# Optimization experiments

Hardware: AMD Instinct MI355X
Metric: run time of the kernel (lower is better)

## Reference

```python
import jax, jax.numpy as jnp
import numpy as np

V, E, H, L, S, B = 32000, 1024, 512, 2, 512, 32  # vocab, emb dim, per-dir hidden, layers, seq, batch
PAD = 0
assert E == 2 * H  # required by the module's pred_emb shape assert; lets cell weights stack


def setup_inputs() -> dict:
    ks = iter(jax.random.split(jax.random.key(0), 40))
    def nrm(shape, scale=0.05):
        return jax.random.normal(next(ks), shape, dtype=jnp.float32) * scale
    seq_input = jax.random.randint(next(ks), (S, B), 1, V)
    # lengths sorted descending (pack_padded convention the torch code assumes)
    lengths = jnp.sort(jax.random.randint(next(ks), (B,), S // 2, S + 1))[::-1]
    inp = {"seq_input": seq_input, "lengths": lengths}
    for name in ("emb1", "emb2", "emb3"):
        inp[name] = nrm((V, E)).at[PAD].set(0.0)  # padding_idx row is zero
    inp["W_et"] = nrm((H, E)); inp["b_et"] = nrm((H,))      # embedding_transform
    inp["W_ct"] = nrm((H, H)); inp["b_ct"] = nrm((H,))      # context_transform
    inp["W_sc"] = nrm((1, H)); inp["b_sc"] = nrm((1,))      # to_scalar
    inp["W_g"] = nrm((E, 2 * E)); inp["b_g"] = nrm((E,))    # embedding_gate Linear
    inp["h0f"] = jax.random.uniform(next(ks), (H,), jnp.float32)  # torch.rand init params
    inp["c0f"] = jax.random.uniform(next(ks), (H,), jnp.float32)
    inp["h0b"] = jax.random.uniform(next(ks), (H,), jnp.float32)
    inp["c0b"] = jax.random.uniform(next(ks), (H,), jnp.float32)
    # LSTMCell weights: [layer, dir(fwd,bwd), 4H, in]; in==E==2H for all layers
    inp["Wih"] = nrm((L, 2, 4 * H, E))
    inp["Whh"] = nrm((L, 2, 4 * H, H))
    inp["bih"] = nrm((L, 2, 4 * H))
    inp["bhh"] = nrm((L, 2, 4 * H))
    return inp


def _lstm_cell(x, h, c, Wih, Whh, bih, bhh):
    g = x @ Wih.T + h @ Whh.T + bih + bhh
    i, f, gg, o = jnp.split(g, 4, axis=-1)
    c2 = jax.nn.sigmoid(f) * c + jax.nn.sigmoid(i) * jnp.tanh(gg)
    return jax.nn.sigmoid(o) * jnp.tanh(c2), c2


def _reverse_seq(x, lengths):
    # reverse the first `length` timesteps per batch element, keep padding in place
    t = jnp.arange(x.shape[0])[:, None]
    idx = jnp.where(t < lengths[None, :], lengths[None, :] - 1 - t, t)  # [S,B]
    idx = idx.reshape(idx.shape + (1,) * (x.ndim - 2))
    return jnp.take_along_axis(x, jnp.broadcast_to(idx, x.shape), axis=0)


def _cos(a, b):
    n = jnp.sum(a * b, -1)
    d = jnp.maximum(jnp.linalg.norm(a, axis=-1) * jnp.linalg.norm(b, axis=-1), 1e-8)
    return n / d


def _forward(seq_input, lengths, emb1, emb2, emb3, W_et, b_et, W_ct, b_ct, W_sc, b_sc,
             W_g, b_g, h0f, c0f, h0b, c0b, Wih, Whh, bih, bhh):
    Sl, Bn = seq_input.shape
    Hh = Whh.shape[-1]
    nL = Wih.shape[0]
    # active mask at step t: lengths >= t+1 (identical for forward and reversed scans)
    mask = jnp.arange(Sl)[:, None] < lengths[None, :]  # [S,B]
    h0f_b = jnp.broadcast_to(h0f, (Bn, Hh)); c0f_b = jnp.broadcast_to(c0f, (Bn, Hh))
    h0b_b = jnp.broadcast_to(h0b, (Bn, Hh)); c0b_b = jnp.broadcast_to(c0b, (Bn, Hh))
    cell = lambda l, d: (Wih[l, d], Whh[l, d], bih[l, d], bhh[l, d])

    def layer0_scan(tokens, cell_p, h0, c0):
        def step(carry, inp):
            h, c, pen = carry
            tok, m = inp
            e1, e2, e3 = emb1[tok], emb2[tok], emb3[tok]  # [B,E]
            p = (jax.nn.relu(_cos(e1, e2) - 0.3) + jax.nn.relu(_cos(e1, e3) - 0.3)
                 + jax.nn.relu(_cos(e2, e3) - 0.3))
            pen = pen + jnp.sum(jnp.where(m, p, 0.0))
            ctx = h @ W_ct.T + b_ct  # [B,H]
            sc = lambda e: jnp.tanh(e @ W_et.T + b_et + ctx) @ W_sc.T + b_sc  # [B,1]
            w = jax.nn.softmax(jnp.concatenate([sc(e1), sc(e2), sc(e3)], -1), axis=-1)
            x = w[:, :1] * e1 + w[:, 1:2] * e2 + w[:, 2:3] * e3  # attended embedding
            h2, c2 = _lstm_cell(x, h, c, *cell_p)
            mm = m[:, None]
            h = jnp.where(mm, h2, h)
            c = jnp.where(mm, c2, c)
            return (h, c, pen), (jnp.where(mm, h2, 0.0), jnp.where(mm, x, 0.0))
        (hf, cf, pen), (outs, preds) = jax.lax.scan(
            step, (h0, c0, jnp.zeros((), jnp.float32)), (tokens, mask))
        return hf, cf, outs, pen, preds

    def layer_scan(xs, cell_p, h0, c0):
        def step(carry, inp):
            h, c = carry
            x, m = inp
            h2, c2 = _lstm_cell(x, h, c, *cell_p)
            mm = m[:, None]
            return (jnp.where(mm, h2, h), jnp.where(mm, c2, c)), jnp.where(mm, h2, 0.0)
        (hf, cf), outs = jax.lax.scan(step, (h0, c0), (xs, mask))
        return hf, cf, outs

    # layer 0 with embedding attention + cosine penalty
    hF, cF, outF, penF, predF = layer0_scan(seq_input, cell(0, 0), h0f_b, c0f_b)
    hB, cB, outB, penB, predB = layer0_scan(_reverse_seq(seq_input, lengths), cell(0, 1), h0b_b, c0b_b)
    penalty = penF + penB
    predB = _reverse_seq(predB, lengths)
    gate = jax.nn.sigmoid(jnp.concatenate([predF, predB], -1) @ W_g.T + b_g)
    pred_emb = predF * gate + predB * (1.0 - gate)
    x = jnp.concatenate([outF, _reverse_seq(outB, lengths)], -1)  # [S,B,2H]
    hs = [hF, hB]; cs = [cF, cB]
    for l in range(1, nL):
        hF, cF, oF = layer_scan(x, cell(l, 0), h0f_b, c0f_b)
        hB, cB, oB = layer_scan(_reverse_seq(x, lengths), cell(l, 1), h0b_b, c0b_b)
        x = jnp.concatenate([oF, _reverse_seq(oB, lengths)], -1)
        hs += [hF, hB]; cs += [cF, cB]
    final_h = jnp.stack(hs, 0)  # [2L,B,H]
    final_c = jnp.stack(cs, 0)
    return final_h, final_c, x, penalty, pred_emb


def reference(seq_input, lengths, emb1, emb2, emb3, W_et, b_et, W_ct, b_ct, W_sc, b_sc,
              W_g, b_g, h0f, c0f, h0b, c0b, Wih, Whh, bih, bhh):
    return _forward(seq_input, lengths, emb1, emb2, emb3, W_et, b_et, W_ct, b_ct, W_sc,
                    b_sc, W_g, b_g, h0f, c0f, h0b, c0b, Wih, Whh, bih, bhh)
```

## Files before the change

### kernel.cpp

```cpp
#include <hip/hip_runtime.h>

typedef unsigned short u16;
typedef unsigned long long u64;
typedef __bf16 bf16_t;
typedef bf16_t bf16x8 __attribute__((ext_vector_type(8)));
typedef float f32x4 __attribute__((ext_vector_type(4)));

#define DEVFN static __device__ __forceinline__

constexpr int S_ = 512, B_ = 32, H_ = 512, E_ = 1024;
constexpr int SB_ = S_ * B_;

constexpr size_t OUT_FH  = 0;
constexpr size_t OUT_FC  = 65536;
constexpr size_t OUT_X   = 131072;
constexpr size_t OUT_PEN = 16908288;
constexpr size_t OUT_PE  = 16908289;

constexpr size_t WS_SLOTS = 0;
constexpr size_t WS_PEN   = 16384;
constexpr size_t WS_SPART = 16640;
constexpr size_t WS_HG0   = 41216;
constexpr size_t WS_HG1   = 106752;
constexpr size_t WS_WET   = 237824;
constexpr size_t WS_WCT   = 1286400;
constexpr size_t WS_WIH0  = 1810688;
constexpr size_t WS_WHH0  = 10199296;
constexpr size_t WS_WIH1  = 14393600;
constexpr size_t WS_WHH1  = 22782208;
constexpr size_t WS_WG    = 26976512;
constexpr size_t WS_EK    = 31170816;
constexpr size_t WS_ET    = 131834112;
constexpr size_t WS_PREDF = 232497408;
constexpr size_t WS_PREDB = 266051840;
constexpr size_t WS_OUT0F = 299606272;
constexpr size_t WS_OUT0B = 316383488;

DEVFN u16 f2bf(float f) {
  union { float f; unsigned u; } v; v.f = f;
  unsigned u = v.u;
  unsigned r = (u + 0x7fffu + ((u >> 16) & 1u)) >> 16;
  return (u16)r;
}
DEVFN float bf2f(u16 h) {
  union { unsigned u; float f; } v; v.u = ((unsigned)h) << 16;
  return v.f;
}
DEVFN float sigm(float x) { return 1.f / (1.f + __expf(-x)); }
DEVFN float tanh_f(float x) { float e = __expf(2.f * x); return 1.f - 2.f / (e + 1.f); }
DEVFN bf16x8 ld_bf8(const u16* p) { return *reinterpret_cast<const bf16x8*>(p); }
DEVFN f32x4 mfma_bf(bf16x8 a, bf16x8 b, f32x4 c) {
  return __builtin_amdgcn_mfma_f32_16x16x32_bf16(a, b, c, 0, 0, 0);
}
DEVFN void lds_st16(u16* base, int row, int rowBytes, int byteCol, bf16x8 v) {
  *reinterpret_cast<bf16x8*>((char*)base + row * rowBytes + (byteCol ^ ((row & 7) << 4))) = v;
}
DEVFN void lds_st8(u16* base, int row, int rowBytes, int byteCol, u64 v) {
  *reinterpret_cast<u64*>((char*)base + row * rowBytes + (byteCol ^ ((row & 7) << 4))) = v;
}
DEVFN bf16x8 lds_ld16(const u16* base, int row, int rowBytes, int byteCol) {
  return *reinterpret_cast<const bf16x8*>((const char*)base + row * rowBytes + (byteCol ^ ((row & 7) << 4)));
}

DEVFN u64 coh_ld64(const u64* p) {
  return __hip_atomic_load(p, __ATOMIC_RELAXED, __HIP_MEMORY_SCOPE_AGENT);
}
DEVFN void coh_st64(u64* p, u64 v) {
  __hip_atomic_store(p, v, __ATOMIC_RELAXED, __HIP_MEMORY_SCOPE_AGENT);
}
DEVFN void coh_st32(unsigned* p, unsigned v) {
  __hip_atomic_store(p, v, __ATOMIC_RELAXED, __HIP_MEMORY_SCOPE_AGENT);
}

DEVFN void gbar_arrive(unsigned* slots, int r, unsigned target) {
  __syncthreads();
  if (threadIdx.x == 0)
    __hip_atomic_store(slots + r * 16, target, __ATOMIC_RELAXED, __HIP_MEMORY_SCOPE_AGENT);
}
DEVFN void gbar_wait(unsigned* slots, unsigned target) {
  if (threadIdx.x < 64) {
    while (__hip_atomic_load(slots + threadIdx.x * 16, __ATOMIC_RELAXED,
                             __HIP_MEMORY_SCOPE_AGENT) < target)
      __builtin_amdgcn_s_sleep(1);
  }
  __syncthreads();
}
DEVFN void gbar(unsigned* slots, int r, unsigned target) {
  gbar_arrive(slots, r, target);
  gbar_wait(slots, target);
}

__global__ void k_f2bf(const float* __restrict__ src, u16* __restrict__ dst, int n) {
  for (int i = blockIdx.x * blockDim.x + threadIdx.x; i < n; i += gridDim.x * blockDim.x)
    dst[i] = f2bf(src[i]);
}

__global__ __launch_bounds__(256) void k_gather(
    const int* __restrict__ seq, const int* __restrict__ lengths,
    const float* __restrict__ emb1, const float* __restrict__ emb2, const float* __restrict__ emb3,
    u16* __restrict__ eK, float* __restrict__ pen) {
  int s = blockIdx.x;
  int t = s >> 5, b = s & 31;
  int tid = threadIdx.x;
  int tok = seq[s];
  const float4* p1 = (const float4*)(emb1 + (size_t)tok * 1024);
  const float4* p2 = (const float4*)(emb2 + (size_t)tok * 1024);
  const float4* p3 = (const float4*)(emb3 + (size_t)tok * 1024);
  float4 a = p1[tid], c = p2[tid], d = p3[tid];
  size_t rb = (size_t)s * 1024 + tid * 4;
  uint2 pk;
  pk.x = f2bf(a.x) | ((unsigned)f2bf(a.y) << 16); pk.y = f2bf(a.z) | ((unsigned)f2bf(a.w) << 16);
  *(uint2*)(eK + rb) = pk;
  pk.x = f2bf(c.x) | ((unsigned)f2bf(c.y) << 16); pk.y = f2bf(c.z) | ((unsigned)f2bf(c.w) << 16);
  *(uint2*)(eK + (size_t)SB_ * 1024 + rb) = pk;
  pk.x = f2bf(d.x) | ((unsigned)f2bf(d.y) << 16); pk.y = f2bf(d.z) | ((unsigned)f2bf(d.w) << 16);
  *(uint2*)(eK + (size_t)2 * SB_ * 1024 + rb) = pk;
  float v[6];
  v[0] = a.x*c.x + a.y*c.y + a.z*c.z + a.w*c.w;
  v[1] = a.x*d.x + a.y*d.y + a.z*d.z + a.w*d.w;
  v[2] = c.x*d.x + c.y*d.y + c.z*d.z + c.w*d.w;
  v[3] = a.x*a.x + a.y*a.y + a.z*a.z + a.w*a.w;
  v[4] = c.x*c.x + c.y*c.y + c.z*c.z + c.w*c.w;
  v[5] = d.x*d.x + d.y*d.y + d.z*d.z + d.w*d.w;
  for (int i = 0; i < 6; ++i)
    for (int m = 1; m < 64; m <<= 1) v[i] += __shfl_xor(v[i], m);
  __shared__ float red[4][6];
  int wid = tid >> 6, lane = tid & 63;
  if (lane == 0) for (int i = 0; i < 6; ++i) red[wid][i] = v[i];
  __syncthreads();
  if (tid == 0) {
    float r[6];
    for (int i = 0; i < 6; ++i) r[i] = red[0][i] + red[1][i] + red[2][i] + red[3][i];
    float c12 = r[0] / fmaxf(sqrtf(r[3]) * sqrtf(r[4]), 1e-8f);
    float c13 = r[1] / fmaxf(sqrtf(r[3]) * sqrtf(r[5]), 1e-8f);
    float c23 = r[2] / fmaxf(sqrtf(r[4]) * sqrtf(r[5]), 1e-8f);
    float p = fmaxf(c12 - 0.3f, 0.f) + fmaxf(c13 - 0.3f, 0.f) + fmaxf(c23 - 0.3f, 0.f);
    if (t < lengths[b] && p > 0.f) atomicAdd(pen, 2.f * p);
  }
}

__global__ __launch_bounds__(256) void k_gemm_et(
    const u16* __restrict__ A, const u16* __restrict__ Bw,
    const float* __restrict__ bias, float* __restrict__ C) {
  int bm = blockIdx.x % 384, bn = blockIdx.x / 384;
  int m0 = bm * 128, n0 = bn * 128;
  __shared__ u16 sA[128 * 64], sB[128 * 64];
  int tid = threadIdx.x, wid = tid >> 6, lane = tid & 63;
  int wm = wid & 1, wn = wid >> 1;
  f32x4 acc[4][4] = {};
  for (int kb = 0; kb < 16; ++kb) {
    __syncthreads();
    for (int c = tid; c < 1024; c += 256) {
      int row = c >> 3, q = c & 7;
      lds_st16(sA, row, 128, q * 16, ld_bf8(A + (size_t)(m0 + row) * 1024 + kb * 64 + q * 8));
      lds_st16(sB, row, 128, q * 16, ld_bf8(Bw + (size_t)(n0 + row) * 1024 + kb * 64 + q * 8));
    }
    __syncthreads();
    for (int kk = 0; kk < 2; ++kk) {
      bf16x8 af[4], bf[4];
      int bc = kk * 64 + (lane >> 4) * 16;
      for (int i = 0; i < 4; ++i) {
        af[i] = lds_ld16(sA, wm * 64 + i * 16 + (lane & 15), 128, bc);
        bf[i] = lds_ld16(sB, wn * 64 + i * 16 + (lane & 15), 128, bc);
      }
      for (int i = 0; i < 4; ++i)
        for (int j = 0; j < 4; ++j) acc[i][j] = mfma_bf(af[i], bf[j], acc[i][j]);
    }
  }
  for (int i = 0; i < 4; ++i)
    for (int j = 0; j < 4; ++j) {
      int m = m0 + wm * 64 + i * 16 + (lane >> 4) * 4;
      int n = n0 + wn * 64 + j * 16 + (lane & 15);
      float bn_ = bias[n & 511];
      for (int r = 0; r < 4; ++r) C[(size_t)(m + r) * 512 + n] = acc[i][j][r] + bn_;
    }
}

__global__ __launch_bounds__(256) void k_gemm_gate(
    const u16* __restrict__ pF, const u16* __restrict__ pB, const u16* __restrict__ Wg,
    const float* __restrict__ bias, float* __restrict__ outPE) {
  int bm = blockIdx.x % 128, bn = blockIdx.x / 128;
  int m0 = bm * 128, n0 = bn * 128;
  __shared__ u16 sA[128 * 64], sB[128 * 64];
  int tid = threadIdx.x, wid = tid >> 6, lane = tid & 63;
  int wm = wid & 1, wn = wid >> 1;
  f32x4 acc[4][4] = {};
  for (int kb = 0; kb < 32; ++kb) {
    __syncthreads();
    const u16* Asrc = (kb < 16) ? pF : pB;
    int kof = (kb < 16) ? kb * 64 : (kb - 16) * 64;
    for (int c = tid; c < 1024; c += 256) {
      int row = c >> 3, q = c & 7;
      lds_st16(sA, row, 128, q * 16, ld_bf8(Asrc + (size_t)(m0 + row) * 1024 + kof + q * 8));
      lds_st16(sB, row, 128, q * 16, ld_bf8(Wg + (size_t)(n0 + row) * 2048 + kb * 64 + q * 8));
    }
    __syncthreads();
    for (int kk = 0; kk < 2; ++kk) {
      bf16x8 af[4], bf[4];
      int bc = kk * 64 + (lane >> 4) * 16;
      for (int i = 0; i < 4; ++i) {
        af[i] = lds_ld16(sA, wm * 64 + i * 16 + (lane & 15), 128, bc);
        bf[i] = lds_ld16(sB, wn * 64 + i * 16 + (lane & 15), 128, bc);
      }
      for (int i = 0; i < 4; ++i)
        for (int j = 0; j < 4; ++j) acc[i][j] = mfma_bf(af[i], bf[j], acc[i][j]);
    }
  }
  for (int i = 0; i < 4; ++i)
    for (int j = 0; j < 4; ++j) {
      int m = m0 + wm * 64 + i * 16 + (lane >> 4) * 4;
      int n = n0 + wn * 64 + j * 16 + (lane & 15);
      float bn_ = bias[n];
      for (int r = 0; r < 4; ++r) {
        float g = sigm(acc[i][j][r] + bn_);
        size_t idx = (size_t)(m + r) * 1024 + n;
        float a = bf2f(pF[idx]), b = bf2f(pB[idx]);
        outPE[idx] = a * g + b * (1.f - g);
      }
    }
}

__global__ __launch_bounds__(256, 1) void k_scan0(
    const u16* __restrict__ eK, const float* __restrict__ eT,
    const u16* __restrict__ wIh0, const u16* __restrict__ wHh0, const u16* __restrict__ wCt,
    const float* __restrict__ Wsc, const float* __restrict__ bct,
    const float* __restrict__ bih, const float* __restrict__ bhh,
    const int* __restrict__ lengths,
    const float* __restrict__ h0f, const float* __restrict__ c0f,
    const float* __restrict__ h0b, const float* __restrict__ c0b,
    u16* __restrict__ hg, float* __restrict__ spart,
    u16* __restrict__ out0F, u16* __restrict__ out0B,
    u16* __restrict__ predF, u16* __restrict__ predB,
    float* __restrict__ dout, unsigned* __restrict__ slots) {
  const int dir = blockIdx.x >> 6;
  const int r   = blockIdx.x & 63;
  const int tid = threadIdx.x, wid = tid >> 6, lane = tid & 63;

  const u16* Wih = wIh0 + (size_t)dir * 2048 * 1024;
  const u16* Whh = wHh0 + (size_t)dir * 2048 * 512;
  const float* bi = bih + dir * 2048;
  const float* bh = bhh + dir * 2048;
  u16* out0 = dir ? out0B : out0F;
  u16* predD = dir ? predB : predF;
  const float* h0 = dir ? h0b : h0f;
  const float* c0 = dir ? c0b : c0f;
  u16* myhg = hg + (size_t)dir * 32 * 512;
  float* spartD = spart + (size_t)dir * 3 * 32 * 32;
  unsigned* slotg = slots + dir * 64 * 16;

  __shared__ u16 sWih[32 * 1024];
  __shared__ u16 sWhh[32 * 512];
  __shared__ u16 sH[32 * 512];
  __shared__ u16 sHpub[256];
  __shared__ float sPW[3][32][32];
  __shared__ float sHW[32][32];
  __shared__ float sSK[3][32];
  __shared__ float sWt[32][4];
  __shared__ float sBias[32];

  for (int c = tid; c < 4096; c += 256) {
    int ln = c >> 7, q = c & 127;
    int n = (ln >> 3) * 512 + r * 8 + (ln & 7);
    lds_st16(sWih, ln, 2048, q * 16, ld_bf8(Wih + (size_t)n * 1024 + q * 8));
  }
  for (int c = tid; c < 2048; c += 256) {
    int ln = c >> 6, q = c & 63;
    int n = (ln >> 3) * 512 + r * 8 + (ln & 7);
    lds_st16(sWhh, ln, 1024, q * 16, ld_bf8(Whh + (size_t)n * 512 + q * 8));
  }
  if (tid < 32) {
    int n = (tid >> 3) * 512 + r * 8 + (tid & 7);
    sBias[tid] = bi[n] + bh[n];
  }

  const int pb = tid >> 3, pj = tid & 7;
  const int gj = r * 8 + pj;
  float hreg = h0[gj], creg = c0[gj];
  const int lenb = lengths[pb];
  const int Lmax = lengths[0];

  const int Mt = wid & 1, Nt = wid >> 1;
  const int arow = Mt * 16 + (lane & 15);
  const int lenrow = lengths[arow];
  const int kq = lane >> 4;
  const int colN = Nt * 16 + (lane & 15);
  const bool isctx = (r < 32) && (wid < 2);
  int lctx[4];
  if (isctx)
    for (int reg = 0; reg < 4; ++reg) lctx[reg] = lengths[Mt * 16 + kq * 4 + reg];

  sHpub[tid] = f2bf(hreg);
  __syncthreads();
  if (tid < 64) {
    u64 v = *reinterpret_cast<const u64*>(sHpub + tid * 4);
    coh_st64((u64*)myhg + (size_t)(tid >> 1) * 128 + r * 2 + (tid & 1), v);
  }
  unsigned rnd = 0;
  gbar(slotg, r, ++rnd);

  for (int t = 0; t < Lmax; ++t) {
    const bool last = (t == Lmax - 1);
    {
      const u64* src = (const u64*)myhg;
      u64 hv[16];
#pragma unroll
      for (int i = 0; i < 16; ++i) hv[i] = coh_ld64(src + tid + i * 256);
#pragma unroll
      for (int i = 0; i < 16; ++i) {
        int c = tid + i * 256, row = c >> 7, q = c & 127;
        lds_st8(sH, row, 1024, q * 8, hv[i]);
      }
    }
    __syncthreads();
    {
      f32x4 acc = {0.f, 0.f, 0.f, 0.f};
#pragma unroll 4
      for (int kb = 0; kb < 16; ++kb) {
        bf16x8 a = lds_ld16(sH, arow, 1024, (kb * 32 + kq * 8) * 2);
        bf16x8 b = lds_ld16(sWhh, colN, 1024, (kb * 32 + kq * 8) * 2);
        acc = mfma_bf(a, b, acc);
      }
      int rb = Mt * 16 + kq * 4;
      for (int reg = 0; reg < 4; ++reg) sHW[rb + reg][colN] = acc[reg];
    }
    if (isctx) {
      f32x4 acc = {0.f, 0.f, 0.f, 0.f};
      int j = r * 16 + (lane & 15);
      const u16* Wctp = wCt + (size_t)j * 512;
#pragma unroll 4
      for (int kb = 0; kb < 16; ++kb) {
        bf16x8 a = lds_ld16(sH, arow, 1024, (kb * 32 + kq * 8) * 2);
        bf16x8 b = ld_bf8(Wctp + kb * 32 + kq * 8);
        acc = mfma_bf(a, b, acc);
      }
      float wsc = Wsc[j], bctj = bct[j];
      float part[3][4];
      for (int reg = 0; reg < 4; ++reg) {
        int b = Mt * 16 + kq * 4 + reg;
        int lb = lctx[reg];
        int pos = (dir == 0) ? t : ((t < lb) ? (lb - 1 - t) : t);
        float ctx = acc[reg] + bctj;
        size_t rowoff = (size_t)(pos * 32 + b) * 512 + j;
        for (int k = 0; k < 3; ++k)
          part[k][reg] = tanh_f(eT[(size_t)k * SB_ * 512 + rowoff] + ctx) * wsc;
      }
      for (int k = 0; k < 3; ++k)
        for (int reg = 0; reg < 4; ++reg) {
          float v = part[k][reg];
          v += __shfl_xor(v, 1); v += __shfl_xor(v, 2);
          v += __shfl_xor(v, 4); v += __shfl_xor(v, 8);
          if ((lane & 15) == 0) {
            int b = Mt * 16 + kq * 4 + reg;
            union { float f; unsigned u; } w; w.f = v;
            coh_st32((unsigned*)(spartD + (k * 32 + b) * 32 + r), w.u);
          }
        }
    }
    unsigned rndA = ++rnd;
    gbar_arrive(slotg, r, rndA);
    {
      int posA = (dir == 0) ? t : ((t < lenrow) ? (lenrow - 1 - t) : t);
      size_t ebase = (size_t)(posA * 32 + arow) * 1024;
      for (int k = 0; k < 3; ++k) {
        const u16* Ek = eK + (size_t)k * SB_ * 1024 + ebase;
        f32x4 acc = {0.f, 0.f, 0.f, 0.f};
#pragma unroll 4
        for (int kb = 0; kb < 32; ++kb) {
          bf16x8 a = ld_bf8(Ek + kb * 32 + kq * 8);
          bf16x8 b = lds_ld16(sWih, colN, 2048, (kb * 32 + kq * 8) * 2);
          acc = mfma_bf(a, b, acc);
        }
        int rb = Mt * 16 + kq * 4;
        for (int reg = 0; reg < 4; ++reg) sPW[k][rb + reg][colN] = acc[reg];
      }
    }
    gbar_wait(slotg, rndA);

    if (tid < 96) {
      int k = tid >> 5, b = tid & 31;
      const u64* sp = (const u64*)(spartD + (k * 32 + b) * 32);
      float s = 0.f;
#pragma unroll
      for (int i = 0; i < 16; ++i) {
        union { u64 u; float f[2]; } w; w.u = coh_ld64(sp + i);
        s += w.f[0] + w.f[1];
      }
      sSK[k][b] = s;
    }
    __syncthreads();
    if (tid < 32) {
      float s0 = sSK[0][tid], s1 = sSK[1][tid], s2 = sSK[2][tid];
      float mx = fmaxf(s0, fmaxf(s1, s2));
      float e0 = __expf(s0 - mx), e1 = __expf(s1 - mx), e2 = __expf(s2 - mx);
      float inv = 1.f / (e0 + e1 + e2);
      sWt[tid][0] = e0 * inv; sWt[tid][1] = e1 * inv; sWt[tid][2] = e2 * inv;
    }
    __syncthreads();
    float w0 = sWt[pb][0], w1 = sWt[pb][1], w2 = sWt[pb][2];
    float h2, c2; bool m; int pos;
    {
      float gq[4];
      for (int q = 0; q < 4; ++q) {
        int cl = q * 8 + pj;
        gq[q] = w0 * sPW[0][pb][cl] + w1 * sPW[1][pb][cl] + w2 * sPW[2][pb][cl]
              + sHW[pb][cl] + sBias[cl];
      }
      float ig = sigm(gq[0]), fg = sigm(gq[1]), gg = tanh_f(gq[2]), og = sigm(gq[3]);
      c2 = fg * creg + ig * gg;
      h2 = og * tanh_f(c2);
      m = (t < lenb);
      if (m) { creg = c2; hreg = h2; }
      pos = (dir == 0) ? t : ((t < lenb) ? (lenb - 1 - t) : t);
      sHpub[tid] = f2bf(hreg);
    }
    unsigned rndB = 0;
    if (!last) {
      __syncthreads();
      if (tid < 64) {
        u64 v = *reinterpret_cast<const u64*>(sHpub + tid * 4);
        coh_st64((u64*)myhg + (size_t)(tid >> 1) * 128 + r * 2 + (tid & 1), v);
      }
      rndB = ++rnd;
      gbar_arrive(slotg, r, rndB);
    }
    {
      out0[(size_t)(pos * 32 + pb) * 512 + gj] = f2bf(m ? h2 : 0.f);
      size_t rowb = (size_t)(pos * 32 + pb) * 1024;
      int e0i = r * 16 + (tid & 7) * 2;
      for (int ii = 0; ii < 2; ++ii) {
        int e = e0i + ii;
        float xv = w0 * bf2f(eK[rowb + e])
                 + w1 * bf2f(eK[(size_t)SB_ * 1024 + rowb + e])
                 + w2 * bf2f(eK[(size_t)2 * SB_ * 1024 + rowb + e]);
        predD[rowb + e] = f2bf(m ? xv : 0.f);
      }
    }
    if (!last) gbar_wait(slotg, rndB);
  }

  dout[OUT_FH + ((size_t)dir * 32 + pb) * 512 + gj] = hreg;
  dout[OUT_FC + ((size_t)dir * 32 + pb) * 512 + gj] = creg;
  for (int row = Lmax * 32 + r; row < SB_; row += 64) {
    if (tid < 128) ((u64*)(out0 + (size_t)row * 512))[tid] = 0;
    ((u64*)(predD + (size_t)row * 1024))[tid] = 0;
  }
}

__global__ __launch_bounds__(256, 1) void k_scan1(
    const u16* __restrict__ out0F, const u16* __restrict__ out0B,
    const u16* __restrict__ wIh1, const u16* __restrict__ wHh1,
    const float* __restrict__ bih, const float* __restrict__ bhh,
    const int* __restrict__ lengths,
    const float* __restrict__ h0f, const float* __restrict__ c0f,
    const float* __restrict__ h0b, const float* __restrict__ c0b,
    u16* __restrict__ hg1, float* __restrict__ dout, unsigned* __restrict__ slots) {
  const int dir = blockIdx.x >> 6;
  const int r   = blockIdx.x & 63;
  const int tid = threadIdx.x, wid = tid >> 6, lane = tid & 63;

  const u16* Wih = wIh1 + (size_t)dir * 2048 * 1024;
  const u16* Whh = wHh1 + (size_t)dir * 2048 * 512;
  const float* bi = bih + (2 + dir) * 2048;
  const float* bh = bhh + (2 + dir) * 2048;
  const float* h0 = dir ? h0b : h0f;
  const float* c0 = dir ? c0b : c0f;
  unsigned* slotg = slots + (2 + dir) * 64 * 16;

  __shared__ u16 sWih[32 * 1024];
  __shared__ u16 sWhh[32 * 512];
  __shared__ u16 sH[32 * 512];
  __shared__ u16 sHpub[256];
  __shared__ float sG[32][32];
  __shared__ float sBias[32];

  for (int c = tid; c < 4096; c += 256) {
    int ln = c >> 7, q = c & 127;
    int n = (ln >> 3) * 512 + r * 8 + (ln & 7);
    lds_st16(sWih, ln, 2048, q * 16, ld_bf8(Wih + (size_t)n * 1024 + q * 8));
  }
  for (int c = tid; c < 2048; c += 256) {
    int ln = c >> 6, q = c & 63;
    int n = (ln >> 3) * 512 + r * 8 + (ln & 7);
    lds_st16(sWhh, ln, 1024, q * 16, ld_bf8(Whh + (size_t)n * 512 + q * 8));
  }
  if (tid < 32) {
    int n = (tid >> 3) * 512 + r * 8 + (tid & 7);
    sBias[tid] = bi[n] + bh[n];
  }

  const int pb = tid >> 3, pj = tid & 7;
  const int gj = r * 8 + pj;
  float hreg = h0[gj], creg = c0[gj];
  const int lenb = lengths[pb];
  const int Lmax = lengths[0];
  const int Mt = wid & 1, Nt = wid >> 1;
  const int arow = Mt * 16 + (lane & 15);
  const int lenrow = lengths[arow];
  const int kq = lane >> 4;
  const int colN = Nt * 16 + (lane & 15);

  __syncthreads();
  f32x4 accx = {0.f, 0.f, 0.f, 0.f};
  {
    int posA = (dir == 0) ? 0 : (lenrow - 1);
    size_t rowb = (size_t)(posA * 32 + arow) * 512;
#pragma unroll 4
    for (int kb = 0; kb < 32; ++kb) {
      const u16* Asrc = (kb < 16) ? (out0F + rowb + kb * 32 + kq * 8)
                                  : (out0B + rowb + (kb - 16) * 32 + kq * 8);
      accx = mfma_bf(ld_bf8(Asrc), lds_ld16(sWih, colN, 2048, (kb * 32 + kq * 8) * 2), accx);
    }
  }

  sHpub[tid] = f2bf(hreg);
  __syncthreads();
  if (tid < 64) {
    u64 v = *reinterpret_cast<const u64*>(sHpub + tid * 4);
    coh_st64((u64*)(hg1 + (size_t)(0 * 2 + dir) * 32 * 512) +
             (size_t)(tid >> 1) * 128 + r * 2 + (tid & 1), v);
  }
  unsigned rnd = 0;
  gbar(slotg, r, ++rnd);

  for (int t = 0; t < Lmax; ++t) {
    const bool last = (t == Lmax - 1);
    int buf = t & 1;
    const u16* hsrc = hg1 + (size_t)(buf * 2 + dir) * 32 * 512;
    u16* hdst = hg1 + (size_t)((buf ^ 1) * 2 + dir) * 32 * 512;
    {
      const u64* src = (const u64*)hsrc;
      u64 hv[16];
#pragma unroll
      for (int i = 0; i < 16; ++i) hv[i] = coh_ld64(src + tid + i * 256);
#pragma unroll
      for (int i = 0; i < 16; ++i) {
        int c = tid + i * 256, row = c >> 7, q = c & 127;
        lds_st8(sH, row, 1024, q * 8, hv[i]);
      }
    }
    __syncthreads();
    f32x4 acc = accx;
#pragma unroll 4
    for (int kb = 0; kb < 16; ++kb) {
      bf16x8 a = lds_ld16(sH, arow, 1024, (kb * 32 + kq * 8) * 2);
      bf16x8 b = lds_ld16(sWhh, colN, 1024, (kb * 32 + kq * 8) * 2);
      acc = mfma_bf(a, b, acc);
    }
    {
      int rb = Mt * 16 + kq * 4;
      for (int reg = 0; reg < 4; ++reg) sG[rb + reg][colN] = acc[reg];
    }
    __syncthreads();
    float h2, c2; bool m; int pos;
    {
      float gq[4];
      for (int q = 0; q < 4; ++q) gq[q] = sG[pb][q * 8 + pj] + sBias[q * 8 + pj];
      float ig = sigm(gq[0]), fg = sigm(gq[1]), gg = tanh_f(gq[2]), og = sigm(gq[3]);
      c2 = fg * creg + ig * gg;
      h2 = og * tanh_f(c2);
      m = (t < lenb);
      if (m) { creg = c2; hreg = h2; }
      pos = (dir == 0) ? t : ((t < lenb) ? (lenb - 1 - t) : t);
      sHpub[tid] = f2bf(hreg);
    }
    unsigned rndB = 0;
    if (!last) {
      __syncthreads();
      if (tid < 64) {
        u64 v = *reinterpret_cast<const u64*>(sHpub + tid * 4);
        coh_st64((u64*)hdst + (size_t)(tid >> 1) * 128 + r * 2 + (tid & 1), v);
      }
      rndB = ++rnd;
      gbar_arrive(slotg, r, rndB);
    }
    dout[OUT_X + (size_t)(pos * 32 + pb) * 1024 + dir * 512 + gj] = m ? h2 : 0.f;
    if (!last) {
      int tn = t + 1;
      int posA = (dir == 0) ? tn : ((tn < lenrow) ? (lenrow - 1 - tn) : tn);
      size_t rowb = (size_t)(posA * 32 + arow) * 512;
      f32x4 ax = {0.f, 0.f, 0.f, 0.f};
#pragma unroll 4
      for (int kb = 0; kb < 32; ++kb) {
        const u16* Asrc = (kb < 16) ? (out0F + rowb + kb * 32 + kq * 8)
                                    : (out0B + rowb + (kb - 16) * 32 + kq * 8);
        ax = mfma_bf(ld_bf8(Asrc), lds_ld16(sWih, colN, 2048, (kb * 32 + kq * 8) * 2), ax);
      }
      accx = ax;
      gbar_wait(slotg, rndB);
    }
  }

  dout[OUT_FH + ((size_t)(2 + dir) * 32 + pb) * 512 + gj] = hreg;
  dout[OUT_FC + ((size_t)(2 + dir) * 32 + pb) * 512 + gj] = creg;
  for (int row = Lmax * 32 + r; row < SB_; row += 64) {
    ((u64*)(dout + OUT_X + (size_t)row * 1024 + dir * 512))[tid] = 0;
  }
}

__global__ void k_final(const float* __restrict__ pen, float* __restrict__ dout) {
  if (threadIdx.x == 0 && blockIdx.x == 0) dout[OUT_PEN] = pen[0];
}

extern "C" void kernel_launch(void* const* d_in, const int* in_sizes, int n_in,
                              void* d_out, int out_size, void* d_ws, size_t ws_size,
                              hipStream_t stream) {
  (void)in_sizes; (void)n_in; (void)out_size; (void)ws_size;
  const int*   seq   = (const int*)d_in[0];
  const int*   lens  = (const int*)d_in[1];
  const float* emb1  = (const float*)d_in[2];
  const float* emb2  = (const float*)d_in[3];
  const float* emb3  = (const float*)d_in[4];
  const float* W_et  = (const float*)d_in[5];
  const float* b_et  = (const float*)d_in[6];
  const float* W_ct  = (const float*)d_in[7];
  const float* b_ct  = (const float*)d_in[8];
  const float* W_sc  = (const float*)d_in[9];
  const float* W_g   = (const float*)d_in[11];
  const float* b_g   = (const float*)d_in[12];
  const float* h0f   = (const float*)d_in[13];
  const float* c0f   = (const float*)d_in[14];
  const float* h0b   = (const float*)d_in[15];
  const float* c0b   = (const float*)d_in[16];
  const float* Wih   = (const float*)d_in[17];
  const float* Whh   = (const float*)d_in[18];
  const float* bih   = (const float*)d_in[19];
  const float* bhh   = (const float*)d_in[20];
  float* out = (float*)d_out;
  char* ws = (char*)d_ws;

  unsigned* slots = (unsigned*)(ws + WS_SLOTS);
  float* pen    = (float*)(ws + WS_PEN);
  float* spart  = (float*)(ws + WS_SPART);
  u16* hg0  = (u16*)(ws + WS_HG0);
  u16* hg1  = (u16*)(ws + WS_HG1);
  u16* wEt  = (u16*)(ws + WS_WET);
  u16* wCt  = (u16*)(ws + WS_WCT);
  u16* wIh0 = (u16*)(ws + WS_WIH0);
  u16* wHh0 = (u16*)(ws + WS_WHH0);
  u16* wIh1 = (u16*)(ws + WS_WIH1);
  u16* wHh1 = (u16*)(ws + WS_WHH1);
  u16* wGg  = (u16*)(ws + WS_WG);
  u16* eK   = (u16*)(ws + WS_EK);
  float* eT = (float*)(ws + WS_ET);
  u16* pF   = (u16*)(ws + WS_PREDF);
  u16* pB   = (u16*)(ws + WS_PREDB);
  u16* o0F  = (u16*)(ws + WS_OUT0F);
  u16* o0B  = (u16*)(ws + WS_OUT0B);

  hipMemsetAsync(ws, 0, 16896, stream);

  hipLaunchKernelGGL(k_f2bf, dim3(512), dim3(256), 0, stream, W_et, wEt, 524288);
  hipLaunchKernelGGL(k_f2bf, dim3(512), dim3(256), 0, stream, W_ct, wCt, 262144);
  hipLaunchKernelGGL(k_f2bf, dim3(2048), dim3(256), 0, stream, Wih, wIh0, 4194304);
  hipLaunchKernelGGL(k_f2bf, dim3(2048), dim3(256), 0, stream, Wih + 4194304, wIh1, 4194304);
  hipLaunchKernelGGL(k_f2bf, dim3(1024), dim3(256), 0, stream, Whh, wHh0, 2097152);
  hipLaunchKernelGGL(k_f2bf, dim3(1024), dim3(256), 0, stream, Whh + 2097152, wHh1, 2097152);
  hipLaunchKernelGGL(k_f2bf, dim3(1024), dim3(256), 0, stream, W_g, wGg, 2097152);

  hipLaunchKernelGGL(k_gather, dim3(SB_), dim3(256), 0, stream,
                     seq, lens, emb1, emb2, emb3, eK, pen);
  hipLaunchKernelGGL(k_gemm_et, dim3(1536), dim3(256), 0, stream, eK, wEt, b_et, eT);
  hipLaunchKernelGGL(k_scan0, dim3(128), dim3(256), 0, stream,
                     eK, eT, wIh0, wHh0, wCt, W_sc, b_ct, bih, bhh, lens,
                     h0f, c0f, h0b, c0b, hg0, spart, o0F, o0B, pF, pB, out, slots);
  hipLaunchKernelGGL(k_scan1, dim3(128), dim3(256), 0, stream,
                     o0F, o0B, wIh1, wHh1, bih, bhh, lens,
                     h0f, c0f, h0b, c0b, hg1, out, slots);
  hipLaunchKernelGGL(k_gemm_gate, dim3(1024), dim3(256), 0, stream,
                     pF, pB, wGg, b_g, out + OUT_PE);
  hipLaunchKernelGGL(k_final, dim3(1), dim3(64), 0, stream, pen, out);
}
```

Measured before the change: 14.44 ms.

## Replace block-wide grid barriers with wave-level flag polling and double-buffered hidden state

Both persistent LSTM scan kernels now double-buffer the published hidden state and signal readiness with per-block flags. A single wave polls those flags with a wave-wide all-check instead of full arrive/wait barriers. Each wave now loads its hidden-state A fragments straight from global memory into registers, which drops the LDS staging copy and one __syncthreads per step. The context-score path gets its own staged flag and prefetches the next step's eT values. Together these aim to shorten the serial per-timestep critical path. The cost is more redundant global loads and subtler memory-ordering correctness that depends on vmcnt waits with relaxed atomics.

After: 16.69 ms. 1.16x slower.

```diff
diff --git a/kernel.cpp b/kernel.cpp
--- a/kernel.cpp
+++ b/kernel.cpp
@@ -18,10 +18,10 @@
 constexpr size_t OUT_PE  = 16908289;
 
 constexpr size_t WS_SLOTS = 0;
-constexpr size_t WS_PEN   = 16384;
-constexpr size_t WS_SPART = 16640;
-constexpr size_t WS_HG0   = 41216;
-constexpr size_t WS_HG1   = 106752;
+constexpr size_t WS_STAG  = 4096;
+constexpr size_t WS_PEN   = 6144;
+constexpr size_t WS_SPART = 6400;
+constexpr size_t WS_HG    = 30976;
 constexpr size_t WS_WET   = 237824;
 constexpr size_t WS_WCT   = 1286400;
 constexpr size_t WS_WIH0  = 1810688;
@@ -55,9 +55,6 @@
 DEVFN void lds_st16(u16* base, int row, int rowBytes, int byteCol, bf16x8 v) {
   *reinterpret_cast<bf16x8*>((char*)base + row * rowBytes + (byteCol ^ ((row & 7) << 4))) = v;
 }
-DEVFN void lds_st8(u16* base, int row, int rowBytes, int byteCol, u64 v) {
-  *reinterpret_cast<u64*>((char*)base + row * rowBytes + (byteCol ^ ((row & 7) << 4))) = v;
-}
 DEVFN bf16x8 lds_ld16(const u16* base, int row, int rowBytes, int byteCol) {
   return *reinterpret_cast<const bf16x8*>((const char*)base + row * rowBytes + (byteCol ^ ((row & 7) << 4)));
 }
@@ -68,26 +65,22 @@
 DEVFN void coh_st64(u64* p, u64 v) {
   __hip_atomic_store(p, v, __ATOMIC_RELAXED, __HIP_MEMORY_SCOPE_AGENT);
 }
+DEVFN unsigned coh_ld32(const unsigned* p) {
+  return __hip_atomic_load(p, __ATOMIC_RELAXED, __HIP_MEMORY_SCOPE_AGENT);
+}
 DEVFN void coh_st32(unsigned* p, unsigned v) {
   __hip_atomic_store(p, v, __ATOMIC_RELAXED, __HIP_MEMORY_SCOPE_AGENT);
 }
-
-DEVFN void gbar_arrive(unsigned* slots, int r, unsigned target) {
-  __syncthreads();
-  if (threadIdx.x == 0)
-    __hip_atomic_store(slots + r * 16, target, __ATOMIC_RELAXED, __HIP_MEMORY_SCOPE_AGENT);
-}
-DEVFN void gbar_wait(unsigned* slots, unsigned target) {
-  if (threadIdx.x < 64) {
-    while (__hip_atomic_load(slots + threadIdx.x * 16, __ATOMIC_RELAXED,
-                             __HIP_MEMORY_SCOPE_AGENT) < target)
-      __builtin_amdgcn_s_sleep(1);
-  }
-  __syncthreads();
-}
-DEVFN void gbar(unsigned* slots, int r, unsigned target) {
-  gbar_arrive(slots, r, target);
-  gbar_wait(slots, target);
+DEVFN void wave_vmcnt0() { asm volatile("s_waitcnt vmcnt(0)" ::: "memory"); }
+
+DEVFN void poll64(const unsigned* tags, unsigned target) {
+  int lane = threadIdx.x & 63;
+  for (;;) {
+    unsigned v = coh_ld32(tags + lane * 4);
+    if (__all(v >= target)) break;
+    __builtin_amdgcn_s_sleep(1);
+  }
+  asm volatile("" ::: "memory");
 }
 
 __global__ void k_f2bf(const float* __restrict__ src, u16* __restrict__ dst, int n) {
@@ -231,7 +224,7 @@
     u16* __restrict__ hg, float* __restrict__ spart,
     u16* __restrict__ out0F, u16* __restrict__ out0B,
     u16* __restrict__ predF, u16* __restrict__ predB,
-    float* __restrict__ dout, unsigned* __restrict__ slots) {
+    float* __restrict__ dout, unsigned* __restrict__ slots, unsigned* __restrict__ stag) {
   const int dir = blockIdx.x >> 6;
   const int r   = blockIdx.x & 63;
   const int tid = threadIdx.x, wid = tid >> 6, lane = tid & 63;
@@ -244,13 +237,13 @@
   u16* predD = dir ? predB : predF;
   const float* h0 = dir ? h0b : h0f;
   const float* c0 = dir ? c0b : c0f;
-  u16* myhg = hg + (size_t)dir * 32 * 512;
+  u16* myhg = hg + (size_t)dir * 2 * 32 * 512;
   float* spartD = spart + (size_t)dir * 3 * 32 * 32;
-  unsigned* slotg = slots + dir * 64 * 16;
+  unsigned* slotg = slots + dir * 64 * 4;
+  unsigned* stagD = stag + dir * 64 * 4;
 
   __shared__ u16 sWih[32 * 1024];
   __shared__ u16 sWhh[32 * 512];
-  __shared__ u16 sH[32 * 512];
   __shared__ u16 sHpub[256];
   __shared__ float sPW[3][32][32];
   __shared__ float sHW[32][32];
@@ -291,35 +284,50 @@
 
   sHpub[tid] = f2bf(hreg);
   __syncthreads();
-  if (tid < 64) {
-    u64 v = *reinterpret_cast<const u64*>(sHpub + tid * 4);
-    coh_st64((u64*)myhg + (size_t)(tid >> 1) * 128 + r * 2 + (tid & 1), v);
-  }
-  unsigned rnd = 0;
-  gbar(slotg, r, ++rnd);
+  if (wid == 0) {
+    u64 v = *reinterpret_cast<const u64*>(sHpub + lane * 4);
+    coh_st64((u64*)myhg + (size_t)(lane >> 1) * 128 + r * 2 + (lane & 1), v);
+    wave_vmcnt0();
+    if (lane == 0) coh_st32(slotg + r * 4, 1u);
+  }
+  if (wid == 0) poll64(slotg, 1u);
+  __syncthreads();
+
+  float petU[3][4];
+  if (isctx) {
+    int j = r * 16 + (lane & 15);
+    for (int reg = 0; reg < 4; ++reg) {
+      int b = Mt * 16 + kq * 4 + reg;
+      int lb = lctx[reg];
+      int pos = (dir == 0) ? 0 : (lb - 1);
+      size_t rowoff = (size_t)(pos * 32 + b) * 512 + j;
+      for (int k = 0; k < 3; ++k) petU[k][reg] = eT[(size_t)k * SB_ * 512 + rowoff];
+    }
+  }
 
   for (int t = 0; t < Lmax; ++t) {
     const bool last = (t == Lmax - 1);
-    {
-      const u64* src = (const u64*)myhg;
-      u64 hv[16];
-#pragma unroll
-      for (int i = 0; i < 16; ++i) hv[i] = coh_ld64(src + tid + i * 256);
-#pragma unroll
-      for (int i = 0; i < 16; ++i) {
-        int c = tid + i * 256, row = c >> 7, q = c & 127;
-        lds_st8(sH, row, 1024, q * 8, hv[i]);
-      }
-    }
-    __syncthreads();
+    bf16x8 hf[16];
+    {
+      const u64* hrow = (const u64*)(myhg + (size_t)(t & 1) * 32 * 512) +
+                        (size_t)arow * 128 + kq * 2;
+      u64 lo[16], hi[16];
+#pragma unroll
+      for (int kb = 0; kb < 16; ++kb) {
+        lo[kb] = coh_ld64(hrow + kb * 8);
+        hi[kb] = coh_ld64(hrow + kb * 8 + 1);
+      }
+#pragma unroll
+      for (int kb = 0; kb < 16; ++kb) {
+        union { u64 q[2]; bf16x8 v; } u; u.q[0] = lo[kb]; u.q[1] = hi[kb];
+        hf[kb] = u.v;
+      }
+    }
     {
       f32x4 acc = {0.f, 0.f, 0.f, 0.f};
-#pragma unroll 4
-      for (int kb = 0; kb < 16; ++kb) {
-        bf16x8 a = lds_ld16(sH, arow, 1024, (kb * 32 + kq * 8) * 2);
-        bf16x8 b = lds_ld16(sWhh, colN, 1024, (kb * 32 + kq * 8) * 2);
-        acc = mfma_bf(a, b, acc);
-      }
+#pragma unroll
+      for (int kb = 0; kb < 16; ++kb)
+        acc = mfma_bf(hf[kb], lds_ld16(sWhh, colN, 1024, (kb * 32 + kq * 8) * 2), acc);
       int rb = Mt * 16 + kq * 4;
       for (int reg = 0; reg < 4; ++reg) sHW[rb + reg][colN] = acc[reg];
     }
@@ -327,26 +335,13 @@
       f32x4 acc = {0.f, 0.f, 0.f, 0.f};
       int j = r * 16 + (lane & 15);
       const u16* Wctp = wCt + (size_t)j * 512;
-#pragma unroll 4
-      for (int kb = 0; kb < 16; ++kb) {
-        bf16x8 a = lds_ld16(sH, arow, 1024, (kb * 32 + kq * 8) * 2);
-        bf16x8 b = ld_bf8(Wctp + kb * 32 + kq * 8);
-        acc = mfma_bf(a, b, acc);
-      }
+#pragma unroll
+      for (int kb = 0; kb < 16; ++kb)
+        acc = mfma_bf(hf[kb], ld_bf8(Wctp + kb * 32 + kq * 8), acc);
       float wsc = Wsc[j], bctj = bct[j];
-      float part[3][4];
-      for (int reg = 0; reg < 4; ++reg) {
-        int b = Mt * 16 + kq * 4 + reg;
-        int lb = lctx[reg];
-        int pos = (dir == 0) ? t : ((t < lb) ? (lb - 1 - t) : t);
-        float ctx = acc[reg] + bctj;
-        size_t rowoff = (size_t)(pos * 32 + b) * 512 + j;
-        for (int k = 0; k < 3; ++k)
-          part[k][reg] = tanh_f(eT[(size_t)k * SB_ * 512 + rowoff] + ctx) * wsc;
-      }
       for (int k = 0; k < 3; ++k)
         for (int reg = 0; reg < 4; ++reg) {
-          float v = part[k][reg];
+          float v = tanh_f(petU[k][reg] + acc[reg] + bctj) * wsc;
           v += __shfl_xor(v, 1); v += __shfl_xor(v, 2);
           v += __shfl_xor(v, 4); v += __shfl_xor(v, 8);
           if ((lane & 15) == 0) {
@@ -355,9 +350,21 @@
             coh_st32((unsigned*)(spartD + (k * 32 + b) * 32 + r), w.u);
           }
         }
-    }
-    unsigned rndA = ++rnd;
-    gbar_arrive(slotg, r, rndA);
+      wave_vmcnt0();
+      if (lane == 0) coh_st32(stagD + (r * 2 + Mt) * 4, (unsigned)(t + 1));
+    }
+    float petN[3][4];
+    if (isctx && t + 1 < Lmax) {
+      int j = r * 16 + (lane & 15);
+      for (int reg = 0; reg < 4; ++reg) {
+        int b = Mt * 16 + kq * 4 + reg;
+        int lb = lctx[reg];
+        int tn = t + 1;
+        int pos = (dir == 0) ? tn : ((tn < lb) ? (lb - 1 - tn) : tn);
+        size_t rowoff = (size_t)(pos * 32 + b) * 512 + j;
+        for (int k = 0; k < 3; ++k) petN[k][reg] = eT[(size_t)k * SB_ * 512 + rowoff];
+      }
+    }
     {
       int posA = (dir == 0) ? t : ((t < lenrow) ? (lenrow - 1 - t) : t);
       size_t ebase = (size_t)(posA * 32 + arow) * 1024;
@@ -365,17 +372,14 @@
         const u16* Ek = eK + (size_t)k * SB_ * 1024 + ebase;
         f32x4 acc = {0.f, 0.f, 0.f, 0.f};
 #pragma unroll 4
-        for (int kb = 0; kb < 32; ++kb) {
-          bf16x8 a = ld_bf8(Ek + kb * 32 + kq * 8);
-          bf16x8 b = lds_ld16(sWih, colN, 2048, (kb * 32 + kq * 8) * 2);
-          acc = mfma_bf(a, b, acc);
-        }
+        for (int kb = 0; kb < 32; ++kb)
+          acc = mfma_bf(ld_bf8(Ek + kb * 32 + kq * 8),
+                        lds_ld16(sWih, colN, 2048, (kb * 32 + kq * 8) * 2), acc);
         int rb = Mt * 16 + kq * 4;
         for (int reg = 0; reg < 4; ++reg) sPW[k][rb + reg][colN] = acc[reg];
       }
     }
-    gbar_wait(slotg, rndA);
-
+    if (wid < 2) poll64(stagD, (unsigned)(t + 1));
     if (tid < 96) {
       int k = tid >> 5, b = tid & 31;
       const u64* sp = (const u64*)(spartD + (k * 32 + b) * 32);
@@ -413,15 +417,13 @@
       pos = (dir == 0) ? t : ((t < lenb) ? (lenb - 1 - t) : t);
       sHpub[tid] = f2bf(hreg);
     }
-    unsigned rndB = 0;
-    if (!last) {
-      __syncthreads();
-      if (tid < 64) {
-        u64 v = *reinterpret_cast<const u64*>(sHpub + tid * 4);
-        coh_st64((u64*)myhg + (size_t)(tid >> 1) * 128 + r * 2 + (tid & 1), v);
-      }
-      rndB = ++rnd;
-      gbar_arrive(slotg, r, rndB);
+    __syncthreads();
+    if (!last && wid == 0) {
+      u64 v = *reinterpret_cast<const u64*>(sHpub + lane * 4);
+      coh_st64((u64*)(myhg + (size_t)((t + 1) & 1) * 32 * 512) +
+               (size_t)(lane >> 1) * 128 + r * 2 + (lane & 1), v);
+      wave_vmcnt0();
+      if (lane == 0) coh_st32(slotg + r * 4, (unsigned)(t + 2));
     }
     {
       out0[(size_t)(pos * 32 + pb) * 512 + gj] = f2bf(m ? h2 : 0.f);
@@ -435,7 +437,13 @@
         predD[rowb + e] = f2bf(m ? xv : 0.f);
       }
     }
-    if (!last) gbar_wait(slotg, rndB);
+    if (isctx)
+      for (int k = 0; k < 3; ++k)
+        for (int reg = 0; reg < 4; ++reg) petU[k][reg] = petN[k][reg];
+    if (!last) {
+      if (wid == 0) poll64(slotg, (unsigned)(t + 2));
+      __syncthreads();
+    }
   }
 
   dout[OUT_FH + ((size_t)dir * 32 + pb) * 512 + gj] = hreg;
@@ -453,7 +461,7 @@
     const int* __restrict__ lengths,
     const float* __restrict__ h0f, const float* __restrict__ c0f,
     const float* __restrict__ h0b, const float* __restrict__ c0b,
-    u16* __restrict__ hg1, float* __restrict__ dout, unsigned* __restrict__ slots) {
+    u16* __restrict__ hg, float* __restrict__ dout, unsigned* __restrict__ slots) {
   const int dir = blockIdx.x >> 6;
   const int r   = blockIdx.x & 63;
   const int tid = threadIdx.x, wid = tid >> 6, lane = tid & 63;
@@ -464,11 +472,10 @@
   const float* bh = bhh + (2 + dir) * 2048;
   const float* h0 = dir ? h0b : h0f;
   const float* c0 = dir ? c0b : c0f;
-  unsigned* slotg = slots + (2 + dir) * 64 * 16;
+  unsigned* slotg = slots + (2 + dir) * 64 * 4;
 
   __shared__ u16 sWih[32 * 1024];
   __shared__ u16 sWhh[32 * 512];
-  __shared__ u16 sH[32 * 512];
   __shared__ u16 sHpub[256];
   __shared__ float sG[32][32];
   __shared__ float sBias[32];
@@ -514,38 +521,38 @@
 
   sHpub[tid] = f2bf(hreg);
   __syncthreads();
-  if (tid < 64) {
-    u64 v = *reinterpret_cast<const u64*>(sHpub + tid * 4);
-    coh_st64((u64*)(hg1 + (size_t)(0 * 2 + dir) * 32 * 512) +
-             (size_t)(tid >> 1) * 128 + r * 2 + (tid & 1), v);
-  }
-  unsigned rnd = 0;
-  gbar(slotg, r, ++rnd);
+  if (wid == 0) {
+    u64 v = *reinterpret_cast<const u64*>(sHpub + lane * 4);
+    coh_st64((u64*)(hg + (size_t)(0 * 2 + dir) * 32 * 512) +
+             (size_t)(lane >> 1) * 128 + r * 2 + (lane & 1), v);
+    wave_vmcnt0();
+    if (lane == 0) coh_st32(slotg + r * 4, 1u);
+  }
+  if (wid == 0) poll64(slotg, 1u);
+  __syncthreads();
 
   for (int t = 0; t < Lmax; ++t) {
     const bool last = (t == Lmax - 1);
-    int buf = t & 1;
-    const u16* hsrc = hg1 + (size_t)(buf * 2 + dir) * 32 * 512;
-    u16* hdst = hg1 + (size_t)((buf ^ 1) * 2 + dir) * 32 * 512;
-    {
-      const u64* src = (const u64*)hsrc;
-      u64 hv[16];
-#pragma unroll
-      for (int i = 0; i < 16; ++i) hv[i] = coh_ld64(src + tid + i * 256);
-#pragma unroll
-      for (int i = 0; i < 16; ++i) {
-        int c = tid + i * 256, row = c >> 7, q = c & 127;
-        lds_st8(sH, row, 1024, q * 8, hv[i]);
-      }
-    }
-    __syncthreads();
+    bf16x8 hf[16];
+    {
+      const u64* hrow = (const u64*)(hg + (size_t)((t & 1) * 2 + dir) * 32 * 512) +
+                        (size_t)arow * 128 + kq * 2;
+      u64 lo[16], hi[16];
+#pragma unroll
+      for (int kb = 0; kb < 16; ++kb) {
+        lo[kb] = coh_ld64(hrow + kb * 8);
+        hi[kb] = coh_ld64(hrow + kb * 8 + 1);
+      }
+#pragma unroll
+      for (int kb = 0; kb < 16; ++kb) {
+        union { u64 q[2]; bf16x8 v; } u; u.q[0] = lo[kb]; u.q[1] = hi[kb];
+        hf[kb] = u.v;
+      }
+    }
     f32x4 acc = accx;
-#pragma unroll 4
-    for (int kb = 0; kb < 16; ++kb) {
-      bf16x8 a = lds_ld16(sH, arow, 1024, (kb * 32 + kq * 8) * 2);
-      bf16x8 b = lds_ld16(sWhh, colN, 1024, (kb * 32 + kq * 8) * 2);
-      acc = mfma_bf(a, b, acc);
-    }
+#pragma unroll
+    for (int kb = 0; kb < 16; ++kb)
+      acc = mfma_bf(hf[kb], lds_ld16(sWhh, colN, 1024, (kb * 32 + kq * 8) * 2), acc);
     {
       int rb = Mt * 16 + kq * 4;
       for (int reg = 0; reg < 4; ++reg) sG[rb + reg][colN] = acc[reg];
@@ -563,15 +570,13 @@
       pos = (dir == 0) ? t : ((t < lenb) ? (lenb - 1 - t) : t);
       sHpub[tid] = f2bf(hreg);
     }
-    unsigned rndB = 0;
-    if (!last) {
-      __syncthreads();
-      if (tid < 64) {
-        u64 v = *reinterpret_cast<const u64*>(sHpub + tid * 4);
-        coh_st64((u64*)hdst + (size_t)(tid >> 1) * 128 + r * 2 + (tid & 1), v);
-      }
-      rndB = ++rnd;
-      gbar_arrive(slotg, r, rndB);
+    __syncthreads();
+    if (!last && wid == 0) {
+      u64 v = *reinterpret_cast<const u64*>(sHpub + lane * 4);
+      coh_st64((u64*)(hg + (size_t)(((t + 1) & 1) * 2 + dir) * 32 * 512) +
+               (size_t)(lane >> 1) * 128 + r * 2 + (lane & 1), v);
+      wave_vmcnt0();
+      if (lane == 0) coh_st32(slotg + r * 4, (unsigned)(t + 2));
     }
     dout[OUT_X + (size_t)(pos * 32 + pb) * 1024 + dir * 512 + gj] = m ? h2 : 0.f;
     if (!last) {
@@ -586,7 +591,8 @@
         ax = mfma_bf(ld_bf8(Asrc), lds_ld16(sWih, colN, 2048, (kb * 32 + kq * 8) * 2), ax);
       }
       accx = ax;
-      gbar_wait(slotg, rndB);
+      if (wid == 0) poll64(slotg, (unsigned)(t + 2));
+      __syncthreads();
     }
   }
 
@@ -629,10 +635,10 @@
   char* ws = (char*)d_ws;
 
   unsigned* slots = (unsigned*)(ws + WS_SLOTS);
+  unsigned* stag  = (unsigned*)(ws + WS_STAG);
   float* pen    = (float*)(ws + WS_PEN);
   float* spart  = (float*)(ws + WS_SPART);
-  u16* hg0  = (u16*)(ws + WS_HG0);
-  u16* hg1  = (u16*)(ws + WS_HG1);
+  u16* hgbuf = (u16*)(ws + WS_HG);
   u16* wEt  = (u16*)(ws + WS_WET);
   u16* wCt  = (u16*)(ws + WS_WCT);
   u16* wIh0 = (u16*)(ws + WS_WIH0);
@@ -647,7 +653,7 @@
   u16* o0F  = (u16*)(ws + WS_OUT0F);
   u16* o0B  = (u16*)(ws + WS_OUT0B);
 
-  hipMemsetAsync(ws, 0, 16896, stream);
+  hipMemsetAsync(ws, 0, 6400, stream);
 
   hipLaunchKernelGGL(k_f2bf, dim3(512), dim3(256), 0, stream, W_et, wEt, 524288);
   hipLaunchKernelGGL(k_f2bf, dim3(512), dim3(256), 0, stream, W_ct, wCt, 262144);
@@ -662,10 +668,10 @@
   hipLaunchKernelGGL(k_gemm_et, dim3(1536), dim3(256), 0, stream, eK, wEt, b_et, eT);
   hipLaunchKernelGGL(k_scan0, dim3(128), dim3(256), 0, stream,
                      eK, eT, wIh0, wHh0, wCt, W_sc, b_ct, bih, bhh, lens,
-                     h0f, c0f, h0b, c0b, hg0, spart, o0F, o0B, pF, pB, out, slots);
+                     h0f, c0f, h0b, c0b, hgbuf, spart, o0F, o0B, pF, pB, out, slots, stag);
   hipLaunchKernelGGL(k_scan1, dim3(128), dim3(256), 0, stream,
                      o0F, o0B, wIh1, wHh1, bih, bhh, lens,
-                     h0f, c0f, h0b, c0b, hg1, out, slots);
+                     h0f, c0f, h0b, c0b, hgbuf, out, slots);
   hipLaunchKernelGGL(k_gemm_gate, dim3(1024), dim3(256), 0, stream,
                      pF, pB, wGg, b_g, out + OUT_PE);
   hipLaunchKernelGGL(k_final, dim3(1), dim3(64), 0, stream, pen, out);
```
